# Kernel tuning notes

Measured on AMD Instinct MI355X. Metric: run time of the kernel, lower is better.

Reference implementation:

```python
import jax, jax.numpy as jnp
import numpy as np

CLAMP_MIN = 1e-6
CLAMP_MAX = 1e6


def setup_inputs() -> dict:
    key = jax.random.key(0)
    k1, k2, k3, k4, k5 = jax.random.split(key, 5)
    R, F, K = 4096, 256, 8
    return {
        "x1": jax.random.normal(k1, (R, F), dtype=jnp.float32),
        "x2": jax.random.normal(k2, (R, F), dtype=jnp.float32),
        "sigmas": jax.random.normal(k3, (K,), dtype=jnp.float32) * 100.0,
        "means": jax.random.normal(k4, (K,), dtype=jnp.float32),
        "sigma_parameters": jax.random.normal(k5, (K,), dtype=jnp.float32),
    }


def reference(x1, x2, sigmas, means, sigma_parameters):
    # dist_k[i,j] = sum_f (x1[i,f] - x2[j,f] - mean_k)^2
    #            = ||x1_i - x2_j||^2 - 2*mean_k*sum_f(x1_i - x2_j) + F*mean_k^2
    # Expansion avoids materializing the R x R x F broadcast tensor.
    R, F = x1.shape
    base = (
        jnp.sum(x1 * x1, axis=1)[:, None]
        + jnp.sum(x2 * x2, axis=1)[None, :]
        - 2.0 * (x1 @ x2.T)
    )  # [R, R]
    s = jnp.sum(x1, axis=1)[:, None] - jnp.sum(x2, axis=1)[None, :]  # [R, R]

    mean = means[:, None, None]  # [K,1,1]
    dist = base[None] - 2.0 * mean * s[None] + jnp.float32(F) * mean * mean  # [K,R,R]
    dist = jnp.clip(dist, CLAMP_MIN, CLAMP_MAX)

    kernel_value = jnp.exp(-dist / (2.0 * sigmas[:, None, None] ** 2))  # [K,R,R]
    softmaxed = jax.nn.softmax(kernel_value, axis=2)  # torch softmax(dim=1) per [R,R]

    weights = 1.0 / (sigma_parameters ** 2)
    normalized_weights = jax.nn.softmax(weights)  # softmax over K
    return jnp.sum(softmaxed * normalized_weights[:, None, None], axis=0)  # [R, R]
```

## Files before the change

### kernel.cpp

```cpp
#include <hip/hip_runtime.h>
#include <cmath>

#define R 4096
#define F 256
#define NK 8

typedef _Float16 half8 __attribute__((ext_vector_type(8)));
typedef _Float16 half4v __attribute__((ext_vector_type(4)));
typedef float f32x4 __attribute__((ext_vector_type(4)));

#define LOG2E      1.4426950408889634f
#define LOG2LOG2E  0.5287663729448977f


__global__ __launch_bounds__(256) void prep_kernel(
    const float* __restrict__ x1, const float* __restrict__ x2,
    const float* __restrict__ sigmas, const float* __restrict__ means,
    const float* __restrict__ sigp,
    _Float16* __restrict__ x1h, _Float16* __restrict__ x2h,
    float* __restrict__ rA, float* __restrict__ cB,
    float* __restrict__ S, float* __restrict__ prm)
{
    const int tid  = threadIdx.x;
    const int wid  = tid >> 6;
    const int lane = tid & 63;
    const int row  = blockIdx.x * 4 + wid;

    const float* src; _Float16* dsth; int r; bool isX1;
    if (row < R) { src = x1; dsth = x1h; r = row;     isX1 = true;  }
    else         { src = x2; dsth = x2h; r = row - R; isX1 = false; }

    float4 v = ((const float4*)(src + (size_t)r * F))[lane];
    half4v h = { (_Float16)v.x, (_Float16)v.y, (_Float16)v.z, (_Float16)v.w };
    *(half4v*)(dsth + (size_t)r * F + lane * 4) = h;

    float s = v.x + v.y + v.z + v.w;
    float q = v.x * v.x + v.y * v.y + v.z * v.z + v.w * v.w;
    for (int m = 1; m < 64; m <<= 1) {
        s += __shfl_xor(s, m);
        q += __shfl_xor(q, m);
    }
    if (lane < NK) {
        int k = lane;
        float sg = sigmas[k], m = means[k];
        float c  = -LOG2E / (2.f * sg * sg);
        if (isX1) rA[k * R + r] = c * (q - 2.f * m * s + (float)F * m * m) + LOG2LOG2E;
        else      cB[k * R + r] = c * (q + 2.f * m * s);
    }

    int g = blockIdx.x * 256 + tid;
    if (g < NK * R) S[g] = 0.f;

    if (blockIdx.x == 0 && tid == 0) {
        float w[NK], mx = -1e30f;
        for (int k = 0; k < NK; ++k) { float sp = sigp[k]; w[k] = 1.f / (sp * sp); mx = fmaxf(mx, w[k]); }
        float sum = 0.f;
        for (int k = 0; k < NK; ++k) { w[k] = expf(w[k] - mx); sum += w[k]; }
        for (int k = 0; k < NK; ++k) prm[k] = w[k] / sum;
        for (int k = 0; k < NK; ++k) {
            float sg = sigmas[k];
            prm[8 + k] = LOG2E / (sg * sg);
        }
    }
}

template <int PHASE>
__global__ __launch_bounds__(256, 2) void gemm_kernel(
    const _Float16* __restrict__ Ah, const _Float16* __restrict__ Bh,
    const float* __restrict__ rA, const float* __restrict__ cB,
    const float* __restrict__ prm, float* __restrict__ S, float* __restrict__ out)
{
    constexpr int SK = 72;
    __shared__ _Float16 As[128 * SK];
    __shared__ _Float16 Bs[128 * SK];

    const int tid  = threadIdx.x;
    const int lane = tid & 63;
    const int wid  = tid >> 6;
    const int wm   = wid >> 1, wn = wid & 1;
    const int q    = lane >> 4, m16 = lane & 15;
    const int tm   = blockIdx.y, tn = blockIdx.x;

    f32x4 acc[4][4];
#pragma unroll
    for (int a = 0; a < 4; ++a)
#pragma unroll
        for (int b = 0; b < 4; ++b)
            acc[a][b] = (f32x4){0.f, 0.f, 0.f, 0.f};

    for (int k0 = 0; k0 < F; k0 += 64) {
#pragma unroll
        for (int c = 0; c < 4; ++c) {
            int idx = c * 256 + tid;
            int row = idx >> 3, c8 = (idx & 7) * 8;
            *(uint4*)&As[row * SK + c8] =
                *(const uint4*)&Ah[(size_t)(tm * 128 + row) * F + k0 + c8];
            *(uint4*)&Bs[row * SK + c8] =
                *(const uint4*)&Bh[(size_t)(tn * 128 + row) * F + k0 + c8];
        }
        __syncthreads();
#pragma unroll
        for (int s = 0; s < 2; ++s) {
            half8 a[4], b[4];
#pragma unroll
            for (int mt = 0; mt < 4; ++mt)
                a[mt] = *(const half8*)&As[(wm * 64 + mt * 16 + m16) * SK + s * 32 + q * 8];
#pragma unroll
            for (int nt = 0; nt < 4; ++nt)
                b[nt] = *(const half8*)&Bs[(wn * 64 + nt * 16 + m16) * SK + s * 32 + q * 8];
#pragma unroll
            for (int mt = 0; mt < 4; ++mt)
#pragma unroll
                for (int nt = 0; nt < 4; ++nt)
                    acc[mt][nt] = __builtin_amdgcn_mfma_f32_16x16x32_f16(
                        a[mt], b[nt], acc[mt][nt], 0, 0, 0);
        }
        __syncthreads();
    }

    float g[8], wv[8];
#pragma unroll
    for (int k = 0; k < 8; ++k) g[k] = prm[8 + k];
    if (PHASE == 1) {
#pragma unroll
        for (int k = 0; k < 8; ++k) wv[k] = prm[k];
    }

    int colg[4];
    float colQ[8][4];
#pragma unroll
    for (int nt = 0; nt < 4; ++nt) {
        colg[nt] = tn * 128 + wn * 64 + nt * 16 + m16;
#pragma unroll
        for (int k = 0; k < 8; ++k) colQ[k][nt] = cB[k * R + colg[nt]];
    }

#pragma unroll
    for (int mt = 0; mt < 4; ++mt) {
#pragma unroll
        for (int r = 0; r < 4; ++r) {
            int rowg = tm * 128 + wm * 64 + mt * 16 + q * 4 + r;
            float rAv[8];
#pragma unroll
            for (int k = 0; k < 8; ++k) rAv[k] = rA[k * R + rowg];

            if (PHASE == 0) {
#pragma unroll
                for (int k = 0; k < 8; ++k) {
                    float t = 0.f;
#pragma unroll
                    for (int nt = 0; nt < 4; ++nt) {
                        float tt = fmaf(g[k], acc[mt][nt][r], rAv[k] + colQ[k][nt]);
                        t += __builtin_amdgcn_exp2f(__builtin_amdgcn_exp2f(tt));
                    }
                    t += __shfl_xor(t, 1); t += __shfl_xor(t, 2);
                    t += __shfl_xor(t, 4); t += __shfl_xor(t, 8);
                    if (m16 == 0) atomicAdd(&S[k * R + rowg], t);
                }
            } else {
                float sv[8];
#pragma unroll
                for (int k = 0; k < 8; ++k)
                    sv[k] = wv[k] * __builtin_amdgcn_rcpf(S[k * R + rowg]);
#pragma unroll
                for (int nt = 0; nt < 4; ++nt) {
                    float d = acc[mt][nt][r];
                    float o = 0.f;
#pragma unroll
                    for (int k = 0; k < 8; ++k) {
                        float tt = fmaf(g[k], d, rAv[k] + colQ[k][nt]);
                        o = fmaf(sv[k], __builtin_amdgcn_exp2f(__builtin_amdgcn_exp2f(tt)), o);
                    }
                    __builtin_nontemporal_store(o, &out[(size_t)rowg * R + colg[nt]]);
                }
            }
        }
    }
}

extern "C" void kernel_launch(void* const* d_in, const int* in_sizes, int n_in,
                              void* d_out, int out_size, void* d_ws, size_t ws_size,
                              hipStream_t stream) {
    (void)in_sizes; (void)n_in; (void)out_size; (void)ws_size;
    const float* x1     = (const float*)d_in[0];
    const float* x2     = (const float*)d_in[1];
    const float* sigmas = (const float*)d_in[2];
    const float* means  = (const float*)d_in[3];
    const float* sigp   = (const float*)d_in[4];
    float* out = (float*)d_out;

    char* ws = (char*)d_ws;
    _Float16* x1h = (_Float16*)ws;
    _Float16* x2h = (_Float16*)(ws + 2097152);
    float* S   = (float*)(ws + 4194304);
    float* rA  = (float*)(ws + 4194304 + 131072);
    float* cB  = (float*)(ws + 4194304 + 262144);
    float* prm = (float*)(ws + 4194304 + 393216);

    prep_kernel<<<2048, 256, 0, stream>>>(x1, x2, sigmas, means, sigp,
                                          x1h, x2h, rA, cB, S, prm);
    gemm_kernel<0><<<dim3(32, 32), 256, 0, stream>>>(x1h, x2h, rA, cB, prm, S, out);
    gemm_kernel<1><<<dim3(32, 32), 256, 0, stream>>>(x1h, x2h, rA, cB, prm, S, out);
}
```

Baseline: 179.0 us.

## Fuse two GEMM passes into one cooperative kernel with a grid sync

Replaces the two-pass design, where the fp16 GEMM ran twice (once to accumulate softmax denominators, once to write output), with a single cooperative kernel. It keeps the accumulators in registers across a grid-wide barrier, so the GEMM and the operand loads happen only once. The kernel asks for 4 blocks per CU so that all 1024 blocks can be resident at once. If the occupancy check or the cooperative launch fails, it falls back to the old two-kernel path. The costs are higher register pressure under the tighter launch bound, which risks spills, plus the overhead of the grid sync.

```diff
diff --git a/kernel.cpp b/kernel.cpp
--- a/kernel.cpp
+++ b/kernel.cpp
@@ -1,5 +1,8 @@
 #include <hip/hip_runtime.h>
+#include <hip/hip_cooperative_groups.h>
 #include <cmath>
+
+namespace cg = cooperative_groups;
 
 #define R 4096
 #define F 256
@@ -64,6 +67,143 @@
     }
 }
 
+__global__ __launch_bounds__(256, 4) void fused_kernel(
+    const _Float16* __restrict__ Ah, const _Float16* __restrict__ Bh,
+    const float* __restrict__ rA, const float* __restrict__ cB,
+    const float* __restrict__ prm, float* __restrict__ S, float* __restrict__ out)
+{
+    constexpr int SK = 72;
+    __shared__ _Float16 As[128 * SK];
+    __shared__ _Float16 Bs[128 * SK];
+
+    const int tid  = threadIdx.x;
+    const int lane = tid & 63;
+    const int wid  = tid >> 6;
+    const int wm   = wid >> 1, wn = wid & 1;
+    const int q    = lane >> 4, m16 = lane & 15;
+    const int tm   = blockIdx.y, tn = blockIdx.x;
+
+    f32x4 acc[4][4];
+#pragma unroll
+    for (int a = 0; a < 4; ++a)
+#pragma unroll
+        for (int b = 0; b < 4; ++b)
+            acc[a][b] = (f32x4){0.f, 0.f, 0.f, 0.f};
+
+    for (int k0 = 0; k0 < F; k0 += 64) {
+#pragma unroll
+        for (int c = 0; c < 4; ++c) {
+            int idx = c * 256 + tid;
+            int row = idx >> 3, c8 = (idx & 7) * 8;
+            *(uint4*)&As[row * SK + c8] =
+                *(const uint4*)&Ah[(size_t)(tm * 128 + row) * F + k0 + c8];
+            *(uint4*)&Bs[row * SK + c8] =
+                *(const uint4*)&Bh[(size_t)(tn * 128 + row) * F + k0 + c8];
+        }
+        __syncthreads();
+#pragma unroll
+        for (int s = 0; s < 2; ++s) {
+            half8 a[4], b[4];
+#pragma unroll
+            for (int mt = 0; mt < 4; ++mt)
+                a[mt] = *(const half8*)&As[(wm * 64 + mt * 16 + m16) * SK + s * 32 + q * 8];
+#pragma unroll
+            for (int nt = 0; nt < 4; ++nt)
+                b[nt] = *(const half8*)&Bs[(wn * 64 + nt * 16 + m16) * SK + s * 32 + q * 8];
+#pragma unroll
+            for (int mt = 0; mt < 4; ++mt)
+#pragma unroll
+                for (int nt = 0; nt < 4; ++nt)
+                    acc[mt][nt] = __builtin_amdgcn_mfma_f32_16x16x32_f16(
+                        a[mt], b[nt], acc[mt][nt], 0, 0, 0);
+        }
+        __syncthreads();
+    }
+
+    {
+        float g[8];
+#pragma unroll
+        for (int k = 0; k < 8; ++k) g[k] = prm[8 + k];
+
+        float colQ[8][4];
+#pragma unroll
+        for (int nt = 0; nt < 4; ++nt) {
+            int colg = tn * 128 + wn * 64 + nt * 16 + m16;
+#pragma unroll
+            for (int k = 0; k < 8; ++k) colQ[k][nt] = cB[k * R + colg];
+        }
+
+#pragma unroll
+        for (int mt = 0; mt < 4; ++mt) {
+#pragma unroll
+            for (int r = 0; r < 4; ++r) {
+                int rowg = tm * 128 + wm * 64 + mt * 16 + q * 4 + r;
+                float rAv[8];
+#pragma unroll
+                for (int k = 0; k < 8; ++k) rAv[k] = rA[k * R + rowg];
+#pragma unroll
+                for (int k = 0; k < 8; ++k) {
+                    float t = 0.f;
+#pragma unroll
+                    for (int nt = 0; nt < 4; ++nt) {
+                        float tt = fmaf(g[k], acc[mt][nt][r], rAv[k] + colQ[k][nt]);
+                        t += __builtin_amdgcn_exp2f(__builtin_amdgcn_exp2f(tt));
+                    }
+                    t += __shfl_xor(t, 1); t += __shfl_xor(t, 2);
+                    t += __shfl_xor(t, 4); t += __shfl_xor(t, 8);
+                    if (m16 == 0) atomicAdd(&S[k * R + rowg], t);
+                }
+            }
+        }
+    }
+
+    __threadfence();
+    cg::this_grid().sync();
+
+    {
+        float g[8], wv[8];
+#pragma unroll
+        for (int k = 0; k < 8; ++k) g[k]  = prm[8 + k];
+#pragma unroll
+        for (int k = 0; k < 8; ++k) wv[k] = prm[k];
+
+        int colg[4];
+        float colQ[8][4];
+#pragma unroll
+        for (int nt = 0; nt < 4; ++nt) {
+            colg[nt] = tn * 128 + wn * 64 + nt * 16 + m16;
+#pragma unroll
+            for (int k = 0; k < 8; ++k) colQ[k][nt] = cB[k * R + colg[nt]];
+        }
+
+#pragma unroll
+        for (int mt = 0; mt < 4; ++mt) {
+#pragma unroll
+            for (int r = 0; r < 4; ++r) {
+                int rowg = tm * 128 + wm * 64 + mt * 16 + q * 4 + r;
+                float rAv[8];
+#pragma unroll
+                for (int k = 0; k < 8; ++k) rAv[k] = rA[k * R + rowg];
+                float sv[8];
+#pragma unroll
+                for (int k = 0; k < 8; ++k)
+                    sv[k] = wv[k] * __builtin_amdgcn_rcpf(S[k * R + rowg]);
+#pragma unroll
+                for (int nt = 0; nt < 4; ++nt) {
+                    float d = acc[mt][nt][r];
+                    float o = 0.f;
+#pragma unroll
+                    for (int k = 0; k < 8; ++k) {
+                        float tt = fmaf(g[k], d, rAv[k] + colQ[k][nt]);
+                        o = fmaf(sv[k], __builtin_amdgcn_exp2f(__builtin_amdgcn_exp2f(tt)), o);
+                    }
+                    __builtin_nontemporal_store(o, &out[(size_t)rowg * R + colg[nt]]);
+                }
+            }
+        }
+    }
+}
+
 template <int PHASE>
 __global__ __launch_bounds__(256, 2) void gemm_kernel(
     const _Float16* __restrict__ Ah, const _Float16* __restrict__ Bh,
@@ -199,6 +339,27 @@
 
     prep_kernel<<<2048, 256, 0, stream>>>(x1, x2, sigmas, means, sigp,
                                           x1h, x2h, rA, cB, S, prm);
-    gemm_kernel<0><<<dim3(32, 32), 256, 0, stream>>>(x1h, x2h, rA, cB, prm, S, out);
-    gemm_kernel<1><<<dim3(32, 32), 256, 0, stream>>>(x1h, x2h, rA, cB, prm, S, out);
+
+    static int coop_state = -1;
+    if (coop_state < 0) {
+        int mb = 0;
+        hipError_t e = hipOccupancyMaxActiveBlocksPerMultiprocessor(
+            &mb, fused_kernel, 256, 0);
+        coop_state = (e == hipSuccess && mb >= 4) ? 1 : 0;
+    }
+
+    bool done = false;
+    if (coop_state == 1) {
+        const _Float16* Ah = x1h; const _Float16* Bh = x2h;
+        void* kargs[] = { (void*)&Ah, (void*)&Bh, (void*)&rA, (void*)&cB,
+                          (void*)&prm, (void*)&S, (void*)&out };
+        hipError_t e = hipLaunchCooperativeKernel(
+            fused_kernel, dim3(32, 32), dim3(256), kargs, 0, stream);
+        if (e == hipSuccess) done = true;
+        else coop_state = 0;
+    }
+    if (!done) {
+        gemm_kernel<0><<<dim3(32, 32), 256, 0, stream>>>(x1h, x2h, rA, cB, prm, S, out);
+        gemm_kernel<1><<<dim3(32, 32), 256, 0, stream>>>(x1h, x2h, rA, cB, prm, S, out);
+    }
 }
```

Result: no change. 181.0 us (+1.1%).

## Store GEMM results to output and finalize in a separate elementwise kernel

Applied to the files above, without the earlier changes.

Instead of recomputing the fp16 GEMM in a second pass, the first pass writes raw dot products into the output buffer while accumulating softmax denominators. A new elementwise finalize kernel reads those values back, applies the kernel/softmax mixture, and writes the result with vectorized coalesced stores. This removes the second GEMM and its tile loads. In exchange it adds a full extra write and read of the R x R output.

```diff
diff --git a/kernel.cpp b/kernel.cpp
--- a/kernel.cpp
+++ b/kernel.cpp
@@ -64,8 +64,7 @@
     }
 }
 
-template <int PHASE>
-__global__ __launch_bounds__(256, 2) void gemm_kernel(
+__global__ __launch_bounds__(256, 2) void gemm_phase0(
     const _Float16* __restrict__ Ah, const _Float16* __restrict__ Bh,
     const float* __restrict__ rA, const float* __restrict__ cB,
     const float* __restrict__ prm, float* __restrict__ S, float* __restrict__ out)
@@ -118,13 +117,9 @@
         __syncthreads();
     }
 
-    float g[8], wv[8];
+    float g[8];
 #pragma unroll
     for (int k = 0; k < 8; ++k) g[k] = prm[8 + k];
-    if (PHASE == 1) {
-#pragma unroll
-        for (int k = 0; k < 8; ++k) wv[k] = prm[k];
-    }
 
     int colg[4];
     float colQ[8][4];
@@ -140,41 +135,68 @@
 #pragma unroll
         for (int r = 0; r < 4; ++r) {
             int rowg = tm * 128 + wm * 64 + mt * 16 + q * 4 + r;
+
+#pragma unroll
+            for (int nt = 0; nt < 4; ++nt)
+                __builtin_nontemporal_store(acc[mt][nt][r],
+                                            &out[(size_t)rowg * R + colg[nt]]);
+
             float rAv[8];
 #pragma unroll
             for (int k = 0; k < 8; ++k) rAv[k] = rA[k * R + rowg];
-
-            if (PHASE == 0) {
-#pragma unroll
-                for (int k = 0; k < 8; ++k) {
-                    float t = 0.f;
-#pragma unroll
-                    for (int nt = 0; nt < 4; ++nt) {
-                        float tt = fmaf(g[k], acc[mt][nt][r], rAv[k] + colQ[k][nt]);
-                        t += __builtin_amdgcn_exp2f(__builtin_amdgcn_exp2f(tt));
-                    }
-                    t += __shfl_xor(t, 1); t += __shfl_xor(t, 2);
-                    t += __shfl_xor(t, 4); t += __shfl_xor(t, 8);
-                    if (m16 == 0) atomicAdd(&S[k * R + rowg], t);
+#pragma unroll
+            for (int k = 0; k < 8; ++k) {
+                float t = 0.f;
+#pragma unroll
+                for (int nt = 0; nt < 4; ++nt) {
+                    float tt = fmaf(g[k], acc[mt][nt][r], rAv[k] + colQ[k][nt]);
+                    t += __builtin_amdgcn_exp2f(__builtin_amdgcn_exp2f(tt));
                 }
-            } else {
-                float sv[8];
-#pragma unroll
-                for (int k = 0; k < 8; ++k)
-                    sv[k] = wv[k] * __builtin_amdgcn_rcpf(S[k * R + rowg]);
-#pragma unroll
-                for (int nt = 0; nt < 4; ++nt) {
-                    float d = acc[mt][nt][r];
-                    float o = 0.f;
-#pragma unroll
-                    for (int k = 0; k < 8; ++k) {
-                        float tt = fmaf(g[k], d, rAv[k] + colQ[k][nt]);
-                        o = fmaf(sv[k], __builtin_amdgcn_exp2f(__builtin_amdgcn_exp2f(tt)), o);
-                    }
-                    __builtin_nontemporal_store(o, &out[(size_t)rowg * R + colg[nt]]);
-                }
+                t += __shfl_xor(t, 1); t += __shfl_xor(t, 2);
+                t += __shfl_xor(t, 4); t += __shfl_xor(t, 8);
+                if (m16 == 0) atomicAdd(&S[k * R + rowg], t);
             }
         }
+    }
+}
+
+__global__ __launch_bounds__(256) void finalize_kernel(
+    const float* __restrict__ rA, const float* __restrict__ cB,
+    const float* __restrict__ prm, const float* __restrict__ S,
+    float* __restrict__ out)
+{
+    const int lane = threadIdx.x & 63;
+    const int w    = threadIdx.x >> 6;
+    const int i0   = blockIdx.y * 64 + w * 16;
+    const int j0   = blockIdx.x * 256 + lane * 4;
+
+    float g[8], wk[8];
+#pragma unroll
+    for (int k = 0; k < 8; ++k) { g[k] = prm[8 + k]; wk[k] = prm[k]; }
+
+    f32x4 cb[8];
+#pragma unroll
+    for (int k = 0; k < 8; ++k) cb[k] = *(const f32x4*)&cB[k * R + j0];
+
+    for (int r = 0; r < 16; ++r) {
+        int i = i0 + r;
+        float ra[8], sv[8];
+#pragma unroll
+        for (int k = 0; k < 8; ++k) {
+            ra[k] = rA[k * R + i];
+            sv[k] = wk[k] * __builtin_amdgcn_rcpf(S[k * R + i]);
+        }
+        f32x4 d = __builtin_nontemporal_load((const f32x4*)&out[(size_t)i * R + j0]);
+        f32x4 o = (f32x4){0.f, 0.f, 0.f, 0.f};
+#pragma unroll
+        for (int k = 0; k < 8; ++k) {
+#pragma unroll
+            for (int e = 0; e < 4; ++e) {
+                float tt = fmaf(g[k], d[e], ra[k] + cb[k][e]);
+                o[e] = fmaf(sv[k], __builtin_amdgcn_exp2f(__builtin_amdgcn_exp2f(tt)), o[e]);
+            }
+        }
+        __builtin_nontemporal_store(o, (f32x4*)&out[(size_t)i * R + j0]);
     }
 }
 
@@ -199,6 +221,6 @@
 
     prep_kernel<<<2048, 256, 0, stream>>>(x1, x2, sigmas, means, sigp,
                                           x1h, x2h, rA, cB, S, prm);
-    gemm_kernel<0><<<dim3(32, 32), 256, 0, stream>>>(x1h, x2h, rA, cB, prm, S, out);
-    gemm_kernel<1><<<dim3(32, 32), 256, 0, stream>>>(x1h, x2h, rA, cB, prm, S, out);
-}
+    gemm_phase0<<<dim3(32, 32), 256, 0, stream>>>(x1h, x2h, rA, cB, prm, S, out);
+    finalize_kernel<<<dim3(16, 64), 256, 0, stream>>>(rA, cB, prm, S, out);
+}
```

Result: slower. 203.4 us (+13.6%).
